# Performance work log

Measured on AMD Instinct MI355X. Metric: run time of the kernel, lower is better.

Reference implementation:

```python
import jax, jax.numpy as jnp
import numpy as np

N = 50000          # nodes
E = 800000         # edges (before self-loops)
G = 64             # graphs in batch
VOCAB = 10000
EMB = 62
HEADS = 4
C = 64             # per-head channels
NUM_CLASSES = 10
NEG_SLOPE = 0.2


def setup_inputs() -> dict:
    key = jax.random.key(0)
    ks = jax.random.split(key, 24)
    inp = {}
    inp['x_ids'] = jax.random.randint(ks[0], (N,), 0, VOCAB)
    inp['degrees'] = jax.random.uniform(ks[1], (N, 2), dtype=jnp.float32)
    inp['edge_src'] = jax.random.randint(ks[2], (E,), 0, N)
    inp['edge_dst'] = jax.random.randint(ks[3], (E,), 0, N)
    inp['batch'] = jnp.sort(jax.random.randint(ks[4], (N,), 0, G))
    # parameters
    inp['emb'] = jax.random.normal(ks[5], (VOCAB, EMB), dtype=jnp.float32)
    d_in = EMB + 2  # 64
    s = lambda f: 1.0 / np.sqrt(f)
    inp['W1'] = jax.random.normal(ks[6], (HEADS * C, d_in), dtype=jnp.float32) * s(d_in)
    inp['as1'] = jax.random.normal(ks[7], (HEADS, C), dtype=jnp.float32) * s(C)
    inp['ad1'] = jax.random.normal(ks[8], (HEADS, C), dtype=jnp.float32) * s(C)
    inp['b1'] = jnp.zeros((HEADS * C,), dtype=jnp.float32)
    inp['W2'] = jax.random.normal(ks[9], (HEADS * C, HEADS * C), dtype=jnp.float32) * s(HEADS * C)
    inp['as2'] = jax.random.normal(ks[10], (HEADS, C), dtype=jnp.float32) * s(C)
    inp['ad2'] = jax.random.normal(ks[11], (HEADS, C), dtype=jnp.float32) * s(C)
    inp['b2'] = jnp.zeros((HEADS * C,), dtype=jnp.float32)
    inp['W3'] = jax.random.normal(ks[12], (1 * C, HEADS * C), dtype=jnp.float32) * s(HEADS * C)
    inp['as3'] = jax.random.normal(ks[13], (1, C), dtype=jnp.float32) * s(C)
    inp['ad3'] = jax.random.normal(ks[14], (1, C), dtype=jnp.float32) * s(C)
    inp['b3'] = jnp.zeros((C,), dtype=jnp.float32)
    inp['linW'] = jax.random.normal(ks[15], (NUM_CLASSES, C), dtype=jnp.float32) * s(C)
    inp['linb'] = jnp.zeros((NUM_CLASSES,), dtype=jnp.float32)
    return inp


def gat_conv(x, src, dst, W, att_src, att_dst, bias, heads, out_ch, concat):
    n = x.shape[0]
    h = (x @ W.T).reshape(n, heads, out_ch)              # [N,H,C]
    a_src = jnp.sum(h * att_src, axis=-1)                # [N,H]
    a_dst = jnp.sum(h * att_dst, axis=-1)                # [N,H]
    e = jax.nn.leaky_relu(a_src[src] + a_dst[dst], NEG_SLOPE)  # [E,H]
    # segmented softmax over incoming edges of each dst node
    emax = jax.ops.segment_max(e, dst, num_segments=n)
    ex = jnp.exp(e - emax[dst])
    denom = jax.ops.segment_sum(ex, dst, num_segments=n)
    alpha = ex / (denom[dst] + 1e-16)                    # [E,H]
    msg = h[src] * alpha[:, :, None]                     # [E,H,C]
    out = jax.ops.segment_sum(msg, dst, num_segments=n)  # [N,H,C]
    out = out.reshape(n, heads * out_ch) if concat else out.mean(axis=1)
    return out + bias


def reference(x_ids, degrees, edge_src, edge_dst, batch, emb,
              W1, as1, ad1, b1, W2, as2, ad2, b2, W3, as3, ad3, b3, linW, linb):
    n = x_ids.shape[0]
    # add self-loops (PyG GATConv default)
    loop = jnp.arange(n)
    src = jnp.concatenate([edge_src, loop])
    dst = jnp.concatenate([edge_dst, loop])
    x = jnp.concatenate([emb[x_ids], degrees], axis=1)   # [N, EMB+2]
    x = jax.nn.relu(gat_conv(x, src, dst, W1, as1, ad1, b1, HEADS, C, True))
    x = jax.nn.relu(gat_conv(x, src, dst, W2, as2, ad2, b2, HEADS, C, True))
    x = jax.nn.relu(gat_conv(x, src, dst, W3, as3, ad3, b3, 1, C, False))
    # global mean pool over graphs
    sums = jax.ops.segment_sum(x, batch, num_segments=G)                    # [G,C]
    cnts = jax.ops.segment_sum(jnp.ones((n,), x.dtype), batch, num_segments=G)
    pooled = sums / jnp.maximum(cnts, 1.0)[:, None]
    return pooled @ linW.T + linb                         # [G, num_classes]
```

## Files before the change

### kernel.cpp

```cpp
#include <hip/hip_runtime.h>
#include <hip/hip_bf16.h>
#include <cstdint>

#define NEG_SLOPE 0.2f

typedef __bf16 bf16x8 __attribute__((ext_vector_type(8)));
typedef float  f32x4  __attribute__((ext_vector_type(4)));

__device__ __forceinline__ unsigned short f2bf(float f) {
    unsigned int u = __float_as_uint(f);
    u += 0x7fffu + ((u >> 16) & 1u);
    return (unsigned short)(u >> 16);
}
__device__ __forceinline__ float bf2f(unsigned short u) {
    return __uint_as_float((unsigned int)u << 16);
}
__device__ __forceinline__ void fma2(float2& a, float ex, unsigned int u) {
    a.x = fmaf(ex, __uint_as_float(u << 16),         a.x);
    a.y = fmaf(ex, __uint_as_float(u & 0xffff0000u), a.y);
}

__global__ void prep_kernel(const float* __restrict__ W1, int n1,
                            const float* __restrict__ W2, int n2,
                            const float* __restrict__ W3, int n3,
                            unsigned short* __restrict__ w1b, unsigned short* __restrict__ w2b,
                            unsigned short* __restrict__ w3b,
                            const int* __restrict__ ids, const float* __restrict__ degs,
                            const float* __restrict__ emb, unsigned short* __restrict__ x,
                            const int* __restrict__ esrc, const int* __restrict__ edst,
                            int* __restrict__ cnt, int* __restrict__ bucket,
                            int* __restrict__ ovd, int* __restrict__ ovs, int* __restrict__ n_over,
                            const int* __restrict__ batch, int* __restrict__ gcnt,
                            int Nn, int E0, int E2, int G,
                            int bW, int bX, int bH)
{
    int b = blockIdx.x;
    if (b < bW) {
        int i = b * 256 + threadIdx.x;
        if (i < n1) w1b[i] = f2bf(W1[i]);
        int j = i - n1;
        if (j >= 0 && j < n2) w2b[j] = f2bf(W2[j]);
        int k = j - n2;
        if (k >= 0 && k < n3) w3b[k] = f2bf(W3[k]);
    } else if (b < bX) {
        int node = (b - bW) * 4 + (threadIdx.x >> 6);
        int lane = threadIdx.x & 63;
        if (node < Nn) {
            int id = ids[node];
            float v;
            if (lane < 62) v = emb[(size_t)id * 62 + lane];
            else           v = degs[node * 2 + (lane - 62)];
            x[(size_t)node * 64 + lane] = f2bf(v);
        }
    } else if (b < bH) {
        int e = (b - bX) * 256 + threadIdx.x;
        if (e < E2) {
            int s, d;
            if (e < E0) { s = esrc[e]; d = edst[e]; }
            else        { s = d = e - E0; }
            int pos = atomicAdd(&cnt[d], 1);
            if (pos < 64) bucket[(size_t)d * 64 + pos] = s;
            else {
                int o = atomicAdd(n_over, 1);
                ovd[o] = d; ovs[o] = s;
            }
        }
    } else {
        int g = threadIdx.x;
        if (g < G) {
            int lo0 = 0, hi = Nn;
            while (lo0 < hi) { int mid = (lo0 + hi) >> 1; if (batch[mid] < g) lo0 = mid + 1; else hi = mid; }
            int lo1 = lo0; hi = Nn;
            while (lo1 < hi) { int mid = (lo1 + hi) >> 1; if (batch[mid] < g + 1) lo1 = mid + 1; else hi = mid; }
            gcnt[g] = lo1 - lo0;
        }
    }
}

__global__ void gemm_mfma(const unsigned short* __restrict__ X, const unsigned short* __restrict__ Wb,
                          unsigned short* __restrict__ Hout,
                          const float* __restrict__ aSrc, const float* __restrict__ aDst,
                          float* __restrict__ a_s, float* __restrict__ a_d,
                          int Nn, int K, int F)
{
    int wid  = (blockIdx.x * blockDim.x + threadIdx.x) >> 6;
    int lane = threadIdx.x & 63;
    int mtiles = (Nn + 63) >> 6;
    int ftiles = F >> 6;
    if (wid >= mtiles * ftiles) return;
    int ft = wid / mtiles;
    int mt = wid - ft * mtiles;
    int m0 = mt << 6, f0 = ft << 6;
    int r = lane & 15, g = lane >> 4, g4 = g << 2;

    const unsigned short* xrow[4];
#pragma unroll
    for (int ja = 0; ja < 4; ++ja) {
        int row = m0 + ja * 16 + r;
        if (row >= Nn) row = Nn - 1;
        xrow[ja] = X + (size_t)row * K + g * 8;
    }
    const unsigned short* wrow = Wb + (size_t)(f0 + r) * K + g * 8;
    const size_t wstep = (size_t)16 * K;

    f32x4 acc[4][4];
#pragma unroll
    for (int a = 0; a < 4; ++a)
#pragma unroll
        for (int b = 0; b < 4; ++b) acc[a][b] = f32x4{0.f, 0.f, 0.f, 0.f};

    for (int k0 = 0; k0 < K; k0 += 32) {
        bf16x8 av[4], bv[4];
#pragma unroll
        for (int ja = 0; ja < 4; ++ja) av[ja] = *reinterpret_cast<const bf16x8*>(xrow[ja] + k0);
#pragma unroll
        for (int jb = 0; jb < 4; ++jb) bv[jb] = *reinterpret_cast<const bf16x8*>(wrow + jb * wstep + k0);
#pragma unroll
        for (int ja = 0; ja < 4; ++ja)
#pragma unroll
            for (int jb = 0; jb < 4; ++jb)
                acc[ja][jb] = __builtin_amdgcn_mfma_f32_16x16x32_bf16(av[ja], bv[jb], acc[ja][jb], 0, 0, 0);
    }

#pragma unroll
    for (int ja = 0; ja < 4; ++ja)
#pragma unroll
        for (int q = 0; q < 4; ++q) {
            int row = m0 + ja * 16 + g4 + q;
            if (row < Nn) {
#pragma unroll
                for (int jb = 0; jb < 4; ++jb)
                    Hout[(size_t)row * F + f0 + jb * 16 + r] = f2bf(acc[ja][jb][q]);
            }
        }

    float ps[4][4], pd[4][4];
#pragma unroll
    for (int ja = 0; ja < 4; ++ja)
#pragma unroll
        for (int q = 0; q < 4; ++q) { ps[ja][q] = 0.f; pd[ja][q] = 0.f; }
#pragma unroll
    for (int jb = 0; jb < 4; ++jb) {
        float ws_ = aSrc[f0 + jb * 16 + r];
        float wd_ = aDst[f0 + jb * 16 + r];
#pragma unroll
        for (int ja = 0; ja < 4; ++ja)
#pragma unroll
            for (int q = 0; q < 4; ++q) {
                ps[ja][q] += acc[ja][jb][q] * ws_;
                pd[ja][q] += acc[ja][jb][q] * wd_;
            }
    }
#pragma unroll
    for (int off = 1; off < 16; off <<= 1)
#pragma unroll
        for (int ja = 0; ja < 4; ++ja)
#pragma unroll
            for (int q = 0; q < 4; ++q) {
                ps[ja][q] += __shfl_xor(ps[ja][q], off, 64);
                pd[ja][q] += __shfl_xor(pd[ja][q], off, 64);
            }
    if (r == 0) {
        int Hh = F >> 6;
#pragma unroll
        for (int ja = 0; ja < 4; ++ja)
#pragma unroll
            for (int q = 0; q < 4; ++q) {
                int n = m0 + ja * 16 + g4 + q;
                if (n < Nn) {
                    a_s[(size_t)n * Hh + ft] = ps[ja][q];
                    a_d[(size_t)n * Hh + ft] = pd[ja][q];
                }
            }
    }
}

template<int H>
__global__ void aggregate_kernel(const unsigned short* __restrict__ Hb,
                                 const float* __restrict__ a_s, const float* __restrict__ a_d,
                                 const int* __restrict__ cnt, const int* __restrict__ bucket,
                                 const int* __restrict__ ovd, const int* __restrict__ ovs,
                                 const int* __restrict__ n_over,
                                 const float* __restrict__ bias,
                                 unsigned short* __restrict__ out, int Nn)
{
    constexpr int F = H * 64;
    constexpr int VEC = F / 64;
    __shared__ uint2 s_pk[4][64][H];
    int w = threadIdx.x >> 6;
    int node = blockIdx.x * 4 + w;
    int lane = threadIdx.x & 63;
    if (node >= Nn) return;
    int deg = cnt[node];

    float adn[H];
#pragma unroll
    for (int h = 0; h < H; ++h) adn[h] = a_d[(size_t)node * H + h];

    if (deg <= 64) {
        bool act = lane < deg;
        int sn = act ? bucket[(size_t)node * 64 + lane] : 0;
        float v[H];
        if (H == 4) {
            const f32x4 av = *reinterpret_cast<const f32x4*>(a_s + (size_t)sn * 4);
#pragma unroll
            for (int h = 0; h < 4; ++h) {
                float t = av[h] + adn[h];
                t = (t > 0.f) ? t : NEG_SLOPE * t;
                v[h] = act ? t : -1e30f;
            }
        } else {
            float t = a_s[sn] + adn[0];
            t = (t > 0.f) ? t : NEG_SLOPE * t;
            v[0] = act ? t : -1e30f;
        }
        float m[H], e[H], s[H];
#pragma unroll
        for (int h = 0; h < H; ++h) {
            m[h] = v[h];
#pragma unroll
            for (int off = 32; off >= 1; off >>= 1)
                m[h] = fmaxf(m[h], __shfl_xor(m[h], off, 64));
        }
#pragma unroll
        for (int h = 0; h < H; ++h) {
            e[h] = act ? __expf(v[h] - m[h]) : 0.f;
            s[h] = e[h];
#pragma unroll
            for (int off = 32; off >= 1; off >>= 1)
                s[h] += __shfl_xor(s[h], off, 64);
        }

#pragma unroll
        for (int h = 0; h < H; ++h)
            s_pk[w][lane][h] = make_uint2((unsigned int)sn, __float_as_uint(e[h]));
        asm volatile("s_waitcnt lgkmcnt(0)" ::: "memory");

        if (H == 4) {
            int laneq = lane & 15, qtr = lane >> 4, hd = laneq >> 2;
            float2 acc2[8];
#pragma unroll
            for (int k = 0; k < 8; ++k) acc2[k] = make_float2(0.f, 0.f);
            for (int j = 0; j < deg; j += 4) {
                uint2 pk = s_pk[w][j + qtr][hd];
                float ex = __uint_as_float(pk.y);
                const uint4* hp = reinterpret_cast<const uint4*>(Hb + (size_t)pk.x * 256 + laneq * 16);
                uint4 u0 = hp[0];
                uint4 u1 = hp[1];
                fma2(acc2[0], ex, u0.x); fma2(acc2[1], ex, u0.y);
                fma2(acc2[2], ex, u0.z); fma2(acc2[3], ex, u0.w);
                fma2(acc2[4], ex, u1.x); fma2(acc2[5], ex, u1.y);
                fma2(acc2[6], ex, u1.z); fma2(acc2[7], ex, u1.w);
            }
#pragma unroll
            for (int k = 0; k < 8; ++k) {
                acc2[k].x += __shfl_xor(acc2[k].x, 32, 64);
                acc2[k].y += __shfl_xor(acc2[k].y, 32, 64);
                acc2[k].x += __shfl_xor(acc2[k].x, 16, 64);
                acc2[k].y += __shfl_xor(acc2[k].y, 16, 64);
            }
            if (lane < 16) {
                int hd2 = lane >> 2;
                float sh = (hd2 == 0) ? s[0] : (hd2 == 1) ? s[1] : (hd2 == 2) ? s[2] : s[3];
                float inv = 1.f / (sh + 1e-16f);
                unsigned int pk8[8];
#pragma unroll
                for (int k = 0; k < 8; ++k) {
                    float t0 = acc2[k].x * inv + bias[lane * 16 + 2 * k];
                    float t1 = acc2[k].y * inv + bias[lane * 16 + 2 * k + 1];
                    unsigned int lo = f2bf(t0 > 0.f ? t0 : 0.f);
                    unsigned int hi = f2bf(t1 > 0.f ? t1 : 0.f);
                    pk8[k] = lo | (hi << 16);
                }
                uint4* op = reinterpret_cast<uint4*>(out + (size_t)node * 256 + lane * 16);
                op[0] = make_uint4(pk8[0], pk8[1], pk8[2], pk8[3]);
                op[1] = make_uint4(pk8[4], pk8[5], pk8[6], pk8[7]);
            }
        } else {
            int laneo = lane & 7, oct = lane >> 3;
            float2 acc2[4];
#pragma unroll
            for (int k = 0; k < 4; ++k) acc2[k] = make_float2(0.f, 0.f);
            for (int j = 0; j < deg; j += 8) {
                uint2 pk = s_pk[w][j + oct][0];
                float ex = __uint_as_float(pk.y);
                const uint4 u = *reinterpret_cast<const uint4*>(Hb + (size_t)pk.x * 64 + laneo * 8);
                fma2(acc2[0], ex, u.x); fma2(acc2[1], ex, u.y);
                fma2(acc2[2], ex, u.z); fma2(acc2[3], ex, u.w);
            }
#pragma unroll
            for (int k = 0; k < 4; ++k) {
                acc2[k].x += __shfl_xor(acc2[k].x, 32, 64);
                acc2[k].y += __shfl_xor(acc2[k].y, 32, 64);
                acc2[k].x += __shfl_xor(acc2[k].x, 16, 64);
                acc2[k].y += __shfl_xor(acc2[k].y, 16, 64);
                acc2[k].x += __shfl_xor(acc2[k].x, 8, 64);
                acc2[k].y += __shfl_xor(acc2[k].y, 8, 64);
            }
            if (lane < 8) {
                float inv = 1.f / (s[0] + 1e-16f);
                unsigned int pk4[4];
#pragma unroll
                for (int k = 0; k < 4; ++k) {
                    float t0 = acc2[k].x * inv + bias[lane * 8 + 2 * k];
                    float t1 = acc2[k].y * inv + bias[lane * 8 + 2 * k + 1];
                    unsigned int lo = f2bf(t0 > 0.f ? t0 : 0.f);
                    unsigned int hi = f2bf(t1 > 0.f ? t1 : 0.f);
                    pk4[k] = lo | (hi << 16);
                }
                *reinterpret_cast<uint4*>(out + (size_t)node * 64 + lane * 8) =
                    make_uint4(pk4[0], pk4[1], pk4[2], pk4[3]);
            }
        }
        return;
    }

    int nov = *n_over;
    int head = (H == 1) ? 0 : (lane >> 4);
    float m[H], s[H];
#pragma unroll
    for (int h = 0; h < H; ++h) { m[h] = -1e30f; s[h] = 0.f; }
    {
        int sn = bucket[(size_t)node * 64 + lane];
#pragma unroll
        for (int h = 0; h < H; ++h) {
            float t = a_s[(size_t)sn * H + h] + adn[h];
            t = (t > 0.f) ? t : NEG_SLOPE * t;
            m[h] = fmaxf(m[h], t);
        }
    }
    for (int i = lane; i < nov; i += 64) {
        if (ovd[i] != node) continue;
        int sn = ovs[i];
#pragma unroll
        for (int h = 0; h < H; ++h) {
            float t = a_s[(size_t)sn * H + h] + adn[h];
            t = (t > 0.f) ? t : NEG_SLOPE * t;
            m[h] = fmaxf(m[h], t);
        }
    }
#pragma unroll
    for (int off = 32; off >= 1; off >>= 1)
#pragma unroll
        for (int h = 0; h < H; ++h) m[h] = fmaxf(m[h], __shfl_xor(m[h], off, 64));
    {
        int sn = bucket[(size_t)node * 64 + lane];
#pragma unroll
        for (int h = 0; h < H; ++h) {
            float t = a_s[(size_t)sn * H + h] + adn[h];
            t = (t > 0.f) ? t : NEG_SLOPE * t;
            s[h] += __expf(t - m[h]);
        }
    }
    for (int i = lane; i < nov; i += 64) {
        if (ovd[i] != node) continue;
        int sn = ovs[i];
#pragma unroll
        for (int h = 0; h < H; ++h) {
            float t = a_s[(size_t)sn * H + h] + adn[h];
            t = (t > 0.f) ? t : NEG_SLOPE * t;
            s[h] += __expf(t - m[h]);
        }
    }
#pragma unroll
    for (int off = 32; off >= 1; off >>= 1)
#pragma unroll
        for (int h = 0; h < H; ++h) s[h] += __shfl_xor(s[h], off, 64);

    float mh, sh, adh;
    if (H == 1) { mh = m[0]; sh = s[0]; adh = adn[0]; }
    else {
        mh  = (head == 0) ? m[0]   : (head == 1) ? m[1]   : (head == 2) ? m[2]   : m[3];
        sh  = (head == 0) ? s[0]   : (head == 1) ? s[1]   : (head == 2) ? s[2]   : s[3];
        adh = (head == 0) ? adn[0] : (head == 1) ? adn[1] : (head == 2) ? adn[2] : adn[3];
    }
    float inv = 1.f / (sh + 1e-16f);
    float acc[VEC];
#pragma unroll
    for (int k = 0; k < VEC; ++k) acc[k] = 0.f;
    for (int j = 0; j < 64; ++j) {
        int sn = bucket[(size_t)node * 64 + j];
        float t = a_s[(size_t)sn * H + head] + adh;
        t = (t > 0.f) ? t : NEG_SLOPE * t;
        float ex = __expf(t - mh);
        const unsigned short* hp = Hb + (size_t)sn * F + lane * VEC;
#pragma unroll
        for (int k = 0; k < VEC; ++k) acc[k] += ex * bf2f(hp[k]);
    }
    for (int i = 0; i < nov; ++i) {
        if (ovd[i] != node) continue;
        int sn = ovs[i];
        float t = a_s[(size_t)sn * H + head] + adh;
        t = (t > 0.f) ? t : NEG_SLOPE * t;
        float ex = __expf(t - mh);
        const unsigned short* hp = Hb + (size_t)sn * F + lane * VEC;
#pragma unroll
        for (int k = 0; k < VEC; ++k) acc[k] += ex * bf2f(hp[k]);
    }
#pragma unroll
    for (int k = 0; k < VEC; ++k) {
        int f = lane * VEC + k;
        float t = acc[k] * inv + bias[f];
        out[(size_t)node * F + f] = f2bf(t > 0.f ? t : 0.f);
    }
}

__global__ void pool_kernel(const unsigned short* __restrict__ x, const int* __restrict__ batch,
                            float* __restrict__ gsums, int Nn)
{
    int lane = threadIdx.x;
    int n0 = blockIdx.x * 64;
    if (n0 >= Nn) return;
    int nend = min(n0 + 64, Nn);
    float acc = 0.f;
    int gcur = batch[n0];
    for (int n = n0; n < nend; ++n) {
        int g = batch[n];
        if (g != gcur) {
            atomicAdd(&gsums[gcur * 64 + lane], acc);
            acc = 0.f;
            gcur = g;
        }
        acc += bf2f(x[(size_t)n * 64 + lane]);
    }
    atomicAdd(&gsums[gcur * 64 + lane], acc);
}

__global__ void final_kernel(const float* __restrict__ gsums, const int* __restrict__ gcnt,
                             const float* __restrict__ linW, const float* __restrict__ linb,
                             float* __restrict__ out, int G)
{
    int t = threadIdx.x;
    if (t >= G * 10) return;
    int g = t / 10, j = t % 10;
    float cnt = (float)max(gcnt[g], 1);
    float acc = 0.f;
#pragma unroll
    for (int c = 0; c < 64; ++c) acc += gsums[g * 64 + c] * linW[j * 64 + c];
    out[g * 10 + j] = acc / cnt + linb[j];
}

extern "C" void kernel_launch(void* const* d_in, const int* in_sizes, int n_in,
                              void* d_out, int out_size, void* d_ws, size_t ws_size,
                              hipStream_t stream)
{
    const int*   x_ids    = (const int*)d_in[0];
    const float* degrees  = (const float*)d_in[1];
    const int*   edge_src = (const int*)d_in[2];
    const int*   edge_dst = (const int*)d_in[3];
    const int*   batch    = (const int*)d_in[4];
    const float* emb      = (const float*)d_in[5];
    const float* W1  = (const float*)d_in[6];
    const float* as1 = (const float*)d_in[7];
    const float* ad1 = (const float*)d_in[8];
    const float* b1  = (const float*)d_in[9];
    const float* W2  = (const float*)d_in[10];
    const float* as2 = (const float*)d_in[11];
    const float* ad2 = (const float*)d_in[12];
    const float* b2  = (const float*)d_in[13];
    const float* W3  = (const float*)d_in[14];
    const float* as3 = (const float*)d_in[15];
    const float* ad3 = (const float*)d_in[16];
    const float* b3  = (const float*)d_in[17];
    const float* linW = (const float*)d_in[18];
    const float* linb = (const float*)d_in[19];

    const int N  = in_sizes[0];
    const int E0 = in_sizes[2];
    const int E2 = E0 + N;
    const int G  = out_size / 10;
    const int nW1 = in_sizes[6], nW2 = in_sizes[10], nW3 = in_sizes[14];

    char* p = (char*)d_ws;
    size_t off = 0;
    auto take = [&](size_t bytes) {
        void* q = p + off;
        off = (off + bytes + 255) & ~(size_t)255;
        return q;
    };
    unsigned short* xA  = (unsigned short*)take((size_t)N * 256 * 2);
    unsigned short* xB  = (unsigned short*)take((size_t)N * 256 * 2);
    float* a_s     = (float*)take((size_t)N * 4 * 4);
    float* a_d     = (float*)take((size_t)N * 4 * 4);
    int*   cnt     = (int*)take((size_t)(N + 64) * 4);
    int*   n_over  = cnt + N;
    int*   bucket  = (int*)take((size_t)N * 64 * 4);
    int*   ovd     = (int*)take((size_t)E2 * 4);
    int*   ovs     = (int*)take((size_t)E2 * 4);
    float* gsums   = (float*)take((size_t)G * 64 * 4);
    int*   gcnt    = (int*)take((size_t)G * 4);
    unsigned short* w1b = (unsigned short*)take((size_t)nW1 * 2);
    unsigned short* w2b = (unsigned short*)take((size_t)nW2 * 2);
    unsigned short* w3b = (unsigned short*)take((size_t)nW3 * 2);

    hipMemsetAsync(cnt, 0, (size_t)(N + 1) * 4, stream);
    hipMemsetAsync(gsums, 0, (size_t)G * 64 * 4, stream);

    const int nodeBlocks4 = (N + 3) / 4;
    const int edgeBlocks  = (E2 + 255) / 256;

    const int nWtot = nW1 + nW2 + nW3;
    const int bW = (nWtot + 255) / 256;
    const int bX = bW + nodeBlocks4;
    const int bH = bX + edgeBlocks;
    prep_kernel<<<bH + 1, 256, 0, stream>>>(W1, nW1, W2, nW2, W3, nW3, w1b, w2b, w3b,
                                            x_ids, degrees, emb, xA,
                                            edge_src, edge_dst, cnt, bucket, ovd, ovs, n_over,
                                            batch, gcnt,
                                            N, E0, E2, G, bW, bX, bH);

    const int mtiles = (N + 63) / 64;
    auto gemmBlocks = [&](int ftiles) { return (mtiles * ftiles + 3) / 4; };

    gemm_mfma<<<gemmBlocks(4), 256, 0, stream>>>(xA, w1b, xB, as1, ad1, a_s, a_d, N, 64, 256);
    aggregate_kernel<4><<<nodeBlocks4, 256, 0, stream>>>(xB, a_s, a_d, cnt, bucket, ovd, ovs, n_over, b1, xA, N);
    gemm_mfma<<<gemmBlocks(4), 256, 0, stream>>>(xA, w2b, xB, as2, ad2, a_s, a_d, N, 256, 256);
    aggregate_kernel<4><<<nodeBlocks4, 256, 0, stream>>>(xB, a_s, a_d, cnt, bucket, ovd, ovs, n_over, b2, xA, N);
    gemm_mfma<<<gemmBlocks(1), 256, 0, stream>>>(xA, w3b, xB, as3, ad3, a_s, a_d, N, 256, 64);
    aggregate_kernel<1><<<nodeBlocks4, 256, 0, stream>>>(xB, a_s, a_d, cnt, bucket, ovd, ovs, n_over, b3, xA, N);

    pool_kernel<<<(N + 63) / 64, 64, 0, stream>>>(xA, batch, gsums, N);
    final_kernel<<<1, ((G * 10 + 63) / 64) * 64, 0, stream>>>(gsums, gcnt, linW, linb, (float*)d_out, G);
}
```

Before: 372.2 us.

## Move edge bucketing into first GEMM launch and seed self-loops in prep

The edge-to-destination bucketing scatter moves out of the prep kernel and into extra blocks of the layer-1 GEMM launch, so the atomic-heavy scatter runs alongside the MFMA work. Self-loops are now written directly by the node-embedding blocks (cnt=1, first bucket slot = node), which removes the counter memset and the self-loop atomics. Each scatter thread handles four edges with batched loads and atomics to raise memory-level parallelism. The scatter's atomic traffic now competes with the GEMM for bandwidth, and bucket slot order becomes nondeterministic as before.

```diff
diff --git a/kernel.cpp b/kernel.cpp
--- a/kernel.cpp
+++ b/kernel.cpp
@@ -27,12 +27,10 @@
                             unsigned short* __restrict__ w3b,
                             const int* __restrict__ ids, const float* __restrict__ degs,
                             const float* __restrict__ emb, unsigned short* __restrict__ x,
-                            const int* __restrict__ esrc, const int* __restrict__ edst,
                             int* __restrict__ cnt, int* __restrict__ bucket,
-                            int* __restrict__ ovd, int* __restrict__ ovs, int* __restrict__ n_over,
+                            int* __restrict__ n_over,
                             const int* __restrict__ batch, int* __restrict__ gcnt,
-                            int Nn, int E0, int E2, int G,
-                            int bW, int bX, int bH)
+                            int Nn, int G, int bW, int bX)
 {
     int b = blockIdx.x;
     if (b < bW) {
@@ -51,18 +49,9 @@
             if (lane < 62) v = emb[(size_t)id * 62 + lane];
             else           v = degs[node * 2 + (lane - 62)];
             x[(size_t)node * 64 + lane] = f2bf(v);
-        }
-    } else if (b < bH) {
-        int e = (b - bX) * 256 + threadIdx.x;
-        if (e < E2) {
-            int s, d;
-            if (e < E0) { s = esrc[e]; d = edst[e]; }
-            else        { s = d = e - E0; }
-            int pos = atomicAdd(&cnt[d], 1);
-            if (pos < 64) bucket[(size_t)d * 64 + pos] = s;
-            else {
-                int o = atomicAdd(n_over, 1);
-                ovd[o] = d; ovs[o] = s;
+            if (lane == 0) {
+                cnt[node] = 1;
+                bucket[(size_t)node * 64] = node;
             }
         }
     } else {
@@ -74,6 +63,135 @@
             while (lo1 < hi) { int mid = (lo1 + hi) >> 1; if (batch[mid] < g + 1) lo1 = mid + 1; else hi = mid; }
             gcnt[g] = lo1 - lo0;
         }
+        if (threadIdx.x == 255) *n_over = 0;
+    }
+}
+
+__global__ void gemm_scatter(const unsigned short* __restrict__ X, const unsigned short* __restrict__ Wb,
+                             unsigned short* __restrict__ Hout,
+                             const float* __restrict__ aSrc, const float* __restrict__ aDst,
+                             float* __restrict__ a_s, float* __restrict__ a_d,
+                             int Nn, int K, int F, int gemmB,
+                             const int* __restrict__ esrc, const int* __restrict__ edst,
+                             int* __restrict__ cnt, int* __restrict__ bucket,
+                             int* __restrict__ ovd, int* __restrict__ ovs, int* __restrict__ n_over,
+                             int E0)
+{
+    if (blockIdx.x >= gemmB) {
+        int base = (blockIdx.x - gemmB) * 1024 + threadIdx.x;
+        int sv[4], dv[4], pv[4];
+        bool ok[4];
+#pragma unroll
+        for (int k = 0; k < 4; ++k) {
+            int e = base + k * 256;
+            ok[k] = (e < E0);
+            if (ok[k]) { sv[k] = esrc[e]; dv[k] = edst[e]; }
+        }
+#pragma unroll
+        for (int k = 0; k < 4; ++k)
+            if (ok[k]) pv[k] = atomicAdd(&cnt[dv[k]], 1);
+#pragma unroll
+        for (int k = 0; k < 4; ++k) {
+            if (ok[k]) {
+                if (pv[k] < 64) bucket[(size_t)dv[k] * 64 + pv[k]] = sv[k];
+                else {
+                    int o = atomicAdd(n_over, 1);
+                    ovd[o] = dv[k]; ovs[o] = sv[k];
+                }
+            }
+        }
+        return;
+    }
+
+    int wid  = (blockIdx.x * blockDim.x + threadIdx.x) >> 6;
+    int lane = threadIdx.x & 63;
+    int mtiles = (Nn + 63) >> 6;
+    int ftiles = F >> 6;
+    if (wid >= mtiles * ftiles) return;
+    int ft = wid / mtiles;
+    int mt = wid - ft * mtiles;
+    int m0 = mt << 6, f0 = ft << 6;
+    int r = lane & 15, g = lane >> 4, g4 = g << 2;
+
+    const unsigned short* xrow[4];
+#pragma unroll
+    for (int ja = 0; ja < 4; ++ja) {
+        int row = m0 + ja * 16 + r;
+        if (row >= Nn) row = Nn - 1;
+        xrow[ja] = X + (size_t)row * K + g * 8;
+    }
+    const unsigned short* wrow = Wb + (size_t)(f0 + r) * K + g * 8;
+    const size_t wstep = (size_t)16 * K;
+
+    f32x4 acc[4][4];
+#pragma unroll
+    for (int a = 0; a < 4; ++a)
+#pragma unroll
+        for (int b = 0; b < 4; ++b) acc[a][b] = f32x4{0.f, 0.f, 0.f, 0.f};
+
+    for (int k0 = 0; k0 < K; k0 += 32) {
+        bf16x8 av[4], bv[4];
+#pragma unroll
+        for (int ja = 0; ja < 4; ++ja) av[ja] = *reinterpret_cast<const bf16x8*>(xrow[ja] + k0);
+#pragma unroll
+        for (int jb = 0; jb < 4; ++jb) bv[jb] = *reinterpret_cast<const bf16x8*>(wrow + jb * wstep + k0);
+#pragma unroll
+        for (int ja = 0; ja < 4; ++ja)
+#pragma unroll
+            for (int jb = 0; jb < 4; ++jb)
+                acc[ja][jb] = __builtin_amdgcn_mfma_f32_16x16x32_bf16(av[ja], bv[jb], acc[ja][jb], 0, 0, 0);
+    }
+
+#pragma unroll
+    for (int ja = 0; ja < 4; ++ja)
+#pragma unroll
+        for (int q = 0; q < 4; ++q) {
+            int row = m0 + ja * 16 + g4 + q;
+            if (row < Nn) {
+#pragma unroll
+                for (int jb = 0; jb < 4; ++jb)
+                    Hout[(size_t)row * F + f0 + jb * 16 + r] = f2bf(acc[ja][jb][q]);
+            }
+        }
+
+    float ps[4][4], pd[4][4];
+#pragma unroll
+    for (int ja = 0; ja < 4; ++ja)
+#pragma unroll
+        for (int q = 0; q < 4; ++q) { ps[ja][q] = 0.f; pd[ja][q] = 0.f; }
+#pragma unroll
+    for (int jb = 0; jb < 4; ++jb) {
+        float ws_ = aSrc[f0 + jb * 16 + r];
+        float wd_ = aDst[f0 + jb * 16 + r];
+#pragma unroll
+        for (int ja = 0; ja < 4; ++ja)
+#pragma unroll
+            for (int q = 0; q < 4; ++q) {
+                ps[ja][q] += acc[ja][jb][q] * ws_;
+                pd[ja][q] += acc[ja][jb][q] * wd_;
+            }
+    }
+#pragma unroll
+    for (int off = 1; off < 16; off <<= 1)
+#pragma unroll
+        for (int ja = 0; ja < 4; ++ja)
+#pragma unroll
+            for (int q = 0; q < 4; ++q) {
+                ps[ja][q] += __shfl_xor(ps[ja][q], off, 64);
+                pd[ja][q] += __shfl_xor(pd[ja][q], off, 64);
+            }
+    if (r == 0) {
+        int Hh = F >> 6;
+#pragma unroll
+        for (int ja = 0; ja < 4; ++ja)
+#pragma unroll
+            for (int q = 0; q < 4; ++q) {
+                int n = m0 + ja * 16 + g4 + q;
+                if (n < Nn) {
+                    a_s[(size_t)n * Hh + ft] = ps[ja][q];
+                    a_d[(size_t)n * Hh + ft] = pd[ja][q];
+                }
+            }
     }
 }
 
@@ -493,26 +611,27 @@
     unsigned short* w2b = (unsigned short*)take((size_t)nW2 * 2);
     unsigned short* w3b = (unsigned short*)take((size_t)nW3 * 2);
 
-    hipMemsetAsync(cnt, 0, (size_t)(N + 1) * 4, stream);
     hipMemsetAsync(gsums, 0, (size_t)G * 64 * 4, stream);
 
     const int nodeBlocks4 = (N + 3) / 4;
-    const int edgeBlocks  = (E2 + 255) / 256;
 
     const int nWtot = nW1 + nW2 + nW3;
     const int bW = (nWtot + 255) / 256;
     const int bX = bW + nodeBlocks4;
-    const int bH = bX + edgeBlocks;
-    prep_kernel<<<bH + 1, 256, 0, stream>>>(W1, nW1, W2, nW2, W3, nW3, w1b, w2b, w3b,
+    prep_kernel<<<bX + 1, 256, 0, stream>>>(W1, nW1, W2, nW2, W3, nW3, w1b, w2b, w3b,
                                             x_ids, degrees, emb, xA,
-                                            edge_src, edge_dst, cnt, bucket, ovd, ovs, n_over,
-                                            batch, gcnt,
-                                            N, E0, E2, G, bW, bX, bH);
+                                            cnt, bucket, n_over, batch, gcnt,
+                                            N, G, bW, bX);
 
     const int mtiles = (N + 63) / 64;
     auto gemmBlocks = [&](int ftiles) { return (mtiles * ftiles + 3) / 4; };
 
-    gemm_mfma<<<gemmBlocks(4), 256, 0, stream>>>(xA, w1b, xB, as1, ad1, a_s, a_d, N, 64, 256);
+    const int gemmB1   = gemmBlocks(4);
+    const int scatterB = (E0 + 1023) / 1024;
+    gemm_scatter<<<gemmB1 + scatterB, 256, 0, stream>>>(xA, w1b, xB, as1, ad1, a_s, a_d,
+                                                        N, 64, 256, gemmB1,
+                                                        edge_src, edge_dst, cnt, bucket,
+                                                        ovd, ovs, n_over, E0);
     aggregate_kernel<4><<<nodeBlocks4, 256, 0, stream>>>(xB, a_s, a_d, cnt, bucket, ovd, ovs, n_over, b1, xA, N);
     gemm_mfma<<<gemmBlocks(4), 256, 0, stream>>>(xA, w2b, xB, as2, ad2, a_s, a_d, N, 256, 256);
     aggregate_kernel<4><<<nodeBlocks4, 256, 0, stream>>>(xB, a_s, a_d, cnt, bucket, ovd, ovs, n_over, b2, xA, N);
```

New measurement: 331.8 us. 1.12x faster.
